# Kernel optimization log

Hardware: AMD Instinct MI355X
Metric: run time of the kernel (lower is better)

Reference implementation:

```python
import jax, jax.numpy as jnp
import numpy as np

B, N, H, F = 4, 512, 4096, 11008   # batch, seq, hidden, intermediate
L, R, RANK = 1, 16, 16             # layers stored, num adapters, lora rank
SCALE = 0.5                        # lora_scale


def setup_inputs() -> dict:
    key = jax.random.key(0)
    ks = jax.random.split(key, 12)
    nrm = lambda k, shape, fan: (jax.random.normal(k, shape, jnp.float32) * (fan ** -0.5))
    inp = {
        "x": jax.random.normal(ks[0], (B, N, H), jnp.float32),
        "W_gate": nrm(ks[1], (F, H), H),
        "W_up": nrm(ks[2], (F, H), H),
        "W_down": nrm(ks[3], (H, F), F),
        # LoRA tables: [num_layers, num_adapters, rank, in] and [num_layers, num_adapters, out, rank]
        "A_gate": nrm(ks[4], (L, R, RANK, H), H),
        "B_gate": nrm(ks[5], (L, R, F, RANK), RANK),
        "A_up": nrm(ks[6], (L, R, RANK, H), H),
        "B_up": nrm(ks[7], (L, R, F, RANK), RANK),
        "A_down": nrm(ks[8], (L, R, RANK, F), F),
        "B_down": nrm(ks[9], (L, R, H, RANK), RANK),
        "lora_indices": jax.random.randint(ks[10], (B,), 0, R),
        "layer_idx": 0,
    }
    return inp


def reference(x, W_gate, W_up, W_down, A_gate, B_gate, A_up, B_up,
              A_down, B_down, lora_indices, layer_idx):
    def lora_add(base, inp, A, B):
        # gather per-sequence adapter slices, then rank-r batched matmuls
        Ab = A[layer_idx][lora_indices]  # [B, r, in]
        Bb = B[layer_idx][lora_indices]  # [B, out, r]
        t = jnp.einsum('bri,bni->bnr', Ab, inp)        # down-project to rank
        return base + jnp.einsum('bor,bnr->bno', Bb, t) * SCALE

    gate = lora_add(jnp.einsum('bnh,fh->bnf', x, W_gate), x, A_gate, B_gate)
    up = lora_add(jnp.einsum('bnh,fh->bnf', x, W_up), x, A_up, B_up)
    act = jax.nn.silu(gate) * up                        # SwiGLU
    down = lora_add(jnp.einsum('bnf,hf->bnh', act, W_down), act, A_down, B_down)
    return down
```

## Files before the change

kernel.cpp:

```cpp
#include <hip/hip_runtime.h>
#include <hip/hip_bf16.h>

typedef __bf16 bf16x8 __attribute__((ext_vector_type(8)));
typedef float  f32x4  __attribute__((ext_vector_type(4)));
typedef unsigned short u16;

#define GLDS16(gsrc, ldst)                                                        \
  __builtin_amdgcn_global_load_lds(                                               \
      (const __attribute__((address_space(1))) unsigned int*)(gsrc),              \
      (__attribute__((address_space(3))) unsigned int*)(ldst), 16, 0, 0)

#define BAR() __builtin_amdgcn_s_barrier()
#define WAIT_LGKM0() asm volatile("s_waitcnt lgkmcnt(0)" ::: "memory")
#define WAIT_VM4() asm volatile("s_waitcnt vmcnt(4)" ::: "memory")

__device__ __forceinline__ u16 f2b(float f) {
  unsigned int u = __builtin_bit_cast(unsigned int, f);
  u = (u + 0x7fffu + ((u >> 16) & 1u)) >> 16;
  return (u16)u;
}
__device__ __forceinline__ float b2f(u16 b) {
  unsigned int u = ((unsigned int)b) << 16;
  return __builtin_bit_cast(float, u);
}

__global__ __launch_bounds__(256) void cvt_kernel(const float4* __restrict__ in,
                                                  ushort4* __restrict__ out, int n4) {
  int i = blockIdx.x * blockDim.x + threadIdx.x;
  int stride = gridDim.x * blockDim.x;
  for (; i < n4; i += stride) {
    float4 v = in[i];
    ushort4 o;
    o.x = f2b(v.x); o.y = f2b(v.y); o.z = f2b(v.z); o.w = f2b(v.w);
    out[i] = o;
  }
}

__global__ __launch_bounds__(256) void lora_t2(const u16* __restrict__ Xb, int K,
                                               const float* __restrict__ A1,
                                               const float* __restrict__ A2,
                                               const int* __restrict__ lidx,
                                               const int* __restrict__ layer,
                                               u16* __restrict__ t1,
                                               u16* __restrict__ t2) {
  __shared__ float red1[4][64][4];
  __shared__ float red2[4][64][4];
  const int lane = threadIdx.x & 63, wid = threadIdx.x >> 6;
  const int m0 = blockIdx.x * 16;
  const int li = lidx[m0 >> 9];
  const size_t abase = ((size_t)layer[0] * 16 + li) * 16 * (size_t)K;
  const int r = lane & 15, kg = lane >> 4;
  const int Kq = K >> 2, kb = wid * Kq;
  f32x4 acc1 = {0.f, 0.f, 0.f, 0.f}, acc2 = {0.f, 0.f, 0.f, 0.f};
  for (int k0 = kb; k0 < kb + Kq; k0 += 32) {
    bf16x8 a = *(const bf16x8*)&Xb[(size_t)(m0 + r) * K + k0 + kg * 8];
    const float* ap = A1 + abase + (size_t)r * K + k0 + kg * 8;
    float4 f0 = *(const float4*)ap;
    float4 f1 = *(const float4*)(ap + 4);
    bf16x8 b;
    b[0] = (__bf16)f0.x; b[1] = (__bf16)f0.y; b[2] = (__bf16)f0.z; b[3] = (__bf16)f0.w;
    b[4] = (__bf16)f1.x; b[5] = (__bf16)f1.y; b[6] = (__bf16)f1.z; b[7] = (__bf16)f1.w;
    acc1 = __builtin_amdgcn_mfma_f32_16x16x32_bf16(a, b, acc1, 0, 0, 0);
    if (A2) {
      const float* ap2 = A2 + abase + (size_t)r * K + k0 + kg * 8;
      float4 g0 = *(const float4*)ap2;
      float4 g1 = *(const float4*)(ap2 + 4);
      bf16x8 b2;
      b2[0] = (__bf16)g0.x; b2[1] = (__bf16)g0.y; b2[2] = (__bf16)g0.z; b2[3] = (__bf16)g0.w;
      b2[4] = (__bf16)g1.x; b2[5] = (__bf16)g1.y; b2[6] = (__bf16)g1.z; b2[7] = (__bf16)g1.w;
      acc2 = __builtin_amdgcn_mfma_f32_16x16x32_bf16(a, b2, acc2, 0, 0, 0);
    }
  }
#pragma unroll
  for (int j = 0; j < 4; ++j) {
    red1[wid][lane][j] = acc1[j];
    if (A2) red2[wid][lane][j] = acc2[j];
  }
  __syncthreads();
  if (wid == 0) {
#pragma unroll
    for (int j = 0; j < 4; ++j) {
      int m = m0 + kg * 4 + j;
      float v1 = red1[0][lane][j] + red1[1][lane][j] + red1[2][lane][j] + red1[3][lane][j];
      t1[(size_t)m * 16 + r] = f2b(0.5f * v1);
      if (A2) {
        float v2 = red2[0][lane][j] + red2[1][lane][j] + red2[2][lane][j] + red2[3][lane][j];
        t2[(size_t)m * 16 + r] = f2b(0.5f * v2);
      }
    }
  }
}

#define RD_A(dst, buf, mh) do {                                                \
    _Pragma("unroll")                                                          \
    for (int mf_ = 0; mf_ < 4; ++mf_)                                          \
      _Pragma("unroll")                                                        \
      for (int ks_ = 0; ks_ < 2; ++ks_) {                                      \
        int row_ = wm * 128 + (mh) * 64 + mf_ * 16 + lr;                       \
        int sl_ = (ks_ * 4 + kg) ^ rx;                                         \
        dst[mf_][ks_] = *(const bf16x8*)&sA[(buf) * 16384 + row_ * 64 + sl_ * 8]; \
      }                                                                        \
  } while (0)

#define RD_B(dst, buf, nh) do {                                                \
    _Pragma("unroll")                                                          \
    for (int nf_ = 0; nf_ < 2; ++nf_)                                          \
      _Pragma("unroll")                                                        \
      for (int ks_ = 0; ks_ < 2; ++ks_) {                                      \
        int row_ = wn * 64 + (nh) * 32 + nf_ * 16 + lr;                        \
        int sl_ = (ks_ * 4 + kg) ^ rx;                                         \
        dst[nf_][ks_] = *(const bf16x8*)&sB[(buf) * 16384 + row_ * 64 + sl_ * 8]; \
      }                                                                        \
  } while (0)

#define RD_BW(dst, SB, buf) do {                                               \
    _Pragma("unroll")                                                          \
    for (int nf_ = 0; nf_ < 2; ++nf_)                                          \
      _Pragma("unroll")                                                        \
      for (int ks_ = 0; ks_ < 2; ++ks_) {                                      \
        int row_ = wn * 32 + nf_ * 16 + lr;                                    \
        int sl_ = (ks_ * 4 + kg) ^ rx;                                         \
        dst[nf_][ks_] = *(const bf16x8*)&SB[(buf) * 8192 + row_ * 64 + sl_ * 8]; \
      }                                                                        \
  } while (0)

#define MMA_Q(AF, BF, mb, nb) do {                                             \
    __builtin_amdgcn_s_setprio(1);                                             \
    _Pragma("unroll")                                                          \
    for (int mf_ = 0; mf_ < 4; ++mf_)                                          \
      _Pragma("unroll")                                                        \
      for (int nf_ = 0; nf_ < 2; ++nf_)                                        \
        _Pragma("unroll")                                                      \
        for (int ks_ = 0; ks_ < 2; ++ks_)                                      \
          acc[(mb) + mf_][(nb) + nf_] = __builtin_amdgcn_mfma_f32_16x16x32_bf16( \
              AF[mf_][ks_], BF[nf_][ks_], acc[(mb) + mf_][(nb) + nf_], 0, 0, 0); \
    __builtin_amdgcn_s_setprio(0);                                             \
  } while (0)

#define MMA_F(AF, BF, ACC, mb) do {                                            \
    __builtin_amdgcn_s_setprio(1);                                             \
    _Pragma("unroll")                                                          \
    for (int mf_ = 0; mf_ < 4; ++mf_)                                          \
      _Pragma("unroll")                                                        \
      for (int nf_ = 0; nf_ < 2; ++nf_)                                        \
        _Pragma("unroll")                                                      \
        for (int ks_ = 0; ks_ < 2; ++ks_)                                      \
          ACC[(mb) + mf_][nf_] = __builtin_amdgcn_mfma_f32_16x16x32_bf16(      \
              AF[mf_][ks_], BF[nf_][ks_], ACC[(mb) + mf_][nf_], 0, 0, 0);      \
    __builtin_amdgcn_s_setprio(0);                                             \
  } while (0)

#define STAGE_F(buf, half, kt) do {                                            \
    const u16* gs_; u16* ld_;                                                  \
    if ((half) == 0)      { gs_ = Xb + (size_t)m0 * 4096 + (size_t)(kt) * 64;         ld_ = sA  + (buf) * 16384; }        \
    else if ((half) == 1) { gs_ = Xb + (size_t)(m0 + 128) * 4096 + (size_t)(kt) * 64; ld_ = sA  + (buf) * 16384 + 8192; } \
    else if ((half) == 2) { gs_ = Wg + (size_t)n0 * 4096 + (size_t)(kt) * 64;         ld_ = sBG + (buf) * 8192; }         \
    else                  { gs_ = Wu + (size_t)n0 * 4096 + (size_t)(kt) * 64;         ld_ = sBU + (buf) * 8192; }         \
    _Pragma("unroll")                                                          \
    for (int i_ = 0; i_ < 2; ++i_) {                                           \
      int ub_ = (wid << 6) + i_ * 512;                                         \
      int un_ = ub_ + lane;                                                    \
      int ur_ = un_ >> 3, us_ = (un_ & 7) ^ (ur_ & 7);                         \
      GLDS16(gs_ + (size_t)ur_ * 4096 + us_ * 8, ld_ + ub_ * 8);               \
    }                                                                          \
  } while (0)

__global__ __launch_bounds__(512, 2) void gemm_gup_fused(
    const u16* __restrict__ Xb, const u16* __restrict__ Wg, const u16* __restrict__ Wu,
    const u16* __restrict__ tg, const u16* __restrict__ tu,
    const float* __restrict__ Bg, const float* __restrict__ Bu,
    const int* __restrict__ lidx, const int* __restrict__ layer,
    u16* __restrict__ act,
    const float4* __restrict__ Wdf, ushort4* __restrict__ wdb3) {
  constexpr int F = 11008;
  const int b = blockIdx.x;
  if (b >= 704) {
    int i = (b - 704) * 512 + threadIdx.x;
    for (; i < 11272192; i += 256 * 512) {
      float4 v = Wdf[i];
      ushort4 o;
      o.x = f2b(v.x); o.y = f2b(v.y); o.z = f2b(v.z); o.w = f2b(v.w);
      wdb3[i] = o;
    }
    return;
  }
  const int xcd = b & 7, j = b >> 3;
  const int ny = xcd + 8 * (j >> 3);
  const int mx = j & 7;
  if (ny >= 86) return;
  extern __shared__ u16 smem[];
  u16* sA  = smem;
  u16* sBG = smem + 32768;
  u16* sBU = smem + 49152;
  const int tid = threadIdx.x, lane = tid & 63, wid = tid >> 6;
  const int lr = lane & 15, kg = lane >> 4, rx = lr & 7;
  const int wm = wid >> 2, wn = wid & 3;
  const int m0 = mx * 256;
  const int n0 = ny * 128;

  f32x4 accg[8][2] = {}, accu[8][2] = {};
  bf16x8 a0[4][2], a1[4][2], bg[2][2], bu[2][2];

  STAGE_F(0, 0, 0); STAGE_F(0, 1, 0); STAGE_F(0, 2, 0); STAGE_F(0, 3, 0);
  STAGE_F(1, 2, 1); STAGE_F(1, 3, 1);
  WAIT_VM4(); BAR();

#pragma unroll 1
  for (int u = 0; u < 32; ++u) {
    const int ktA = (2 * u + 1) & 63;
    const int kt0 = (2 * u + 2) & 63;
    const int kt1 = (2 * u + 3) & 63;
    RD_A(a0, 0, 0); RD_BW(bg, sBG, 0);
    STAGE_F(1, 0, ktA);
    BAR(); WAIT_LGKM0();
    MMA_F(a0, bg, accg, 0);
    BAR();
    RD_BW(bu, sBU, 0);
    STAGE_F(1, 1, ktA);
    BAR(); WAIT_LGKM0();
    MMA_F(a0, bu, accu, 0);
    BAR();
    RD_A(a1, 0, 1);
    STAGE_F(0, 2, kt0);
    BAR(); WAIT_LGKM0();
    MMA_F(a1, bu, accu, 4);
    BAR();
    STAGE_F(0, 3, kt0);
    BAR();
    MMA_F(a1, bg, accg, 4);
    WAIT_VM4();
    BAR();
    RD_A(a0, 1, 0); RD_BW(bg, sBG, 1);
    STAGE_F(0, 0, kt0);
    BAR(); WAIT_LGKM0();
    MMA_F(a0, bg, accg, 0);
    BAR();
    RD_BW(bu, sBU, 1);
    STAGE_F(0, 1, kt0);
    BAR(); WAIT_LGKM0();
    MMA_F(a0, bu, accu, 0);
    BAR();
    RD_A(a1, 1, 1);
    STAGE_F(1, 2, kt1);
    BAR(); WAIT_LGKM0();
    MMA_F(a1, bu, accu, 4);
    BAR();
    STAGE_F(1, 3, kt1);
    BAR();
    MMA_F(a1, bg, accg, 4);
    WAIT_VM4();
    BAR();
  }

  const int li = lidx[m0 >> 9];
  const size_t bbase = ((size_t)layer[0] * 16 + li) * (size_t)F * 16;
  bf16x8 la[8], lb[2];
  const bf16x8 zz = {};
#pragma unroll
  for (int mf = 0; mf < 8; ++mf) {
    int row = m0 + wm * 128 + mf * 16 + lr;
    la[mf] = (kg < 2) ? *(const bf16x8*)&tg[(size_t)row * 16 + kg * 8] : zz;
  }
#pragma unroll
  for (int nf = 0; nf < 2; ++nf) {
    int col = n0 + wn * 32 + nf * 16 + lr;
    if (kg < 2) {
      const float* bp = Bg + bbase + (size_t)col * 16 + kg * 8;
      float4 f0 = *(const float4*)bp;
      float4 f1 = *(const float4*)(bp + 4);
      bf16x8 v;
      v[0] = (__bf16)f0.x; v[1] = (__bf16)f0.y; v[2] = (__bf16)f0.z; v[3] = (__bf16)f0.w;
      v[4] = (__bf16)f1.x; v[5] = (__bf16)f1.y; v[6] = (__bf16)f1.z; v[7] = (__bf16)f1.w;
      lb[nf] = v;
    } else lb[nf] = zz;
  }
#pragma unroll
  for (int mf = 0; mf < 8; ++mf)
#pragma unroll
    for (int nf = 0; nf < 2; ++nf)
      accg[mf][nf] = __builtin_amdgcn_mfma_f32_16x16x32_bf16(la[mf], lb[nf], accg[mf][nf], 0, 0, 0);
#pragma unroll
  for (int mf = 0; mf < 8; ++mf) {
    int row = m0 + wm * 128 + mf * 16 + lr;
    la[mf] = (kg < 2) ? *(const bf16x8*)&tu[(size_t)row * 16 + kg * 8] : zz;
  }
#pragma unroll
  for (int nf = 0; nf < 2; ++nf) {
    int col = n0 + wn * 32 + nf * 16 + lr;
    if (kg < 2) {
      const float* bp = Bu + bbase + (size_t)col * 16 + kg * 8;
      float4 f0 = *(const float4*)bp;
      float4 f1 = *(const float4*)(bp + 4);
      bf16x8 v;
      v[0] = (__bf16)f0.x; v[1] = (__bf16)f0.y; v[2] = (__bf16)f0.z; v[3] = (__bf16)f0.w;
      v[4] = (__bf16)f1.x; v[5] = (__bf16)f1.y; v[6] = (__bf16)f1.z; v[7] = (__bf16)f1.w;
      lb[nf] = v;
    } else lb[nf] = zz;
  }
#pragma unroll
  for (int mf = 0; mf < 8; ++mf)
#pragma unroll
    for (int nf = 0; nf < 2; ++nf)
      accu[mf][nf] = __builtin_amdgcn_mfma_f32_16x16x32_bf16(la[mf], lb[nf], accu[mf][nf], 0, 0, 0);

#pragma unroll
  for (int mf = 0; mf < 8; ++mf)
#pragma unroll
    for (int nf = 0; nf < 2; ++nf)
#pragma unroll
      for (int j2 = 0; j2 < 4; ++j2) {
        int row = m0 + wm * 128 + mf * 16 + kg * 4 + j2;
        int col = n0 + wn * 32 + nf * 16 + lr;
        float g = accg[mf][nf][j2], uu = accu[mf][nf][j2];
        float s = g / (1.f + __expf(-g));
        act[(size_t)row * F + col] = f2b(s * uu);
      }
}

#define STAGE_D(buf, half, kt) do {                                           \
    int r0_ = ((half) & 1) * 128;                                             \
    const u16* gs_ = ((half) < 2)                                             \
        ? (Ab + (size_t)(m0 + r0_) * 11008 + (size_t)(kt) * 64)               \
        : (Wd + (size_t)(n0 + r0_) * 11008 + (size_t)(kt) * 64);              \
    u16* ld_ = (((half) < 2) ? sA : sB) + (buf) * 16384 + r0_ * 64;           \
    _Pragma("unroll")                                                         \
    for (int i_ = 0; i_ < 2; ++i_) {                                          \
      int ub_ = (wid << 6) + i_ * 512;                                        \
      int un_ = ub_ + lane;                                                   \
      int ur_ = un_ >> 3, us_ = (un_ & 7) ^ (ur_ & 7);                        \
      GLDS16(gs_ + (size_t)ur_ * 11008 + us_ * 8, ld_ + ub_ * 8);             \
    }                                                                         \
  } while (0)

#define KT(t) (kbase + ((t) >= 86 ? (t) - 86 : (t)))

__global__ __launch_bounds__(512, 2) void gemm_down8(
    const u16* __restrict__ Ab, const u16* __restrict__ Wd,
    const u16* __restrict__ td, const float* __restrict__ Bd,
    const int* __restrict__ lidx, const int* __restrict__ layer,
    float* __restrict__ P0, float* __restrict__ P1) {
  constexpr int H = 4096;
  extern __shared__ u16 smem[];
  u16* sA = smem;
  u16* sB = smem + 32768;
  const int tid = threadIdx.x, lane = tid & 63, wid = tid >> 6;
  const int lr = lane & 15, kg = lane >> 4, rx = lr & 7;
  const int wm = wid >> 2, wn = wid & 3;
  const int m0 = blockIdx.x * 256, n0 = blockIdx.y * 256;
  const int kbase = blockIdx.z * 86;
  float* P = blockIdx.z ? P1 : P0;

  f32x4 acc[8][4] = {};
  bf16x8 a0[4][2], a1[4][2], b0[2][2], b1[2][2];

  STAGE_D(0, 0, KT(0)); STAGE_D(0, 1, KT(0)); STAGE_D(0, 2, KT(0)); STAGE_D(0, 3, KT(0));
  STAGE_D(1, 2, KT(1)); STAGE_D(1, 3, KT(1));
  WAIT_VM4(); BAR();

#pragma unroll 1
  for (int u = 0; u < 43; ++u) {
    const int ktA = KT(2 * u + 1);
    const int kt0 = KT(2 * u + 2);
    const int kt1 = KT(2 * u + 3);
    RD_A(a0, 0, 0); RD_B(b0, 0, 0);
    STAGE_D(1, 0, ktA);
    BAR(); WAIT_LGKM0();
    MMA_Q(a0, b0, 0, 0);
    BAR();
    RD_B(b1, 0, 1);
    STAGE_D(1, 1, ktA);
    BAR(); WAIT_LGKM0();
    MMA_Q(a0, b1, 0, 2);
    BAR();
    RD_A(a1, 0, 1);
    STAGE_D(0, 2, kt0);
    BAR(); WAIT_LGKM0();
    MMA_Q(a1, b1, 4, 2);
    BAR();
    STAGE_D(0, 3, kt0);
    BAR();
    MMA_Q(a1, b0, 4, 0);
    WAIT_VM4();
    BAR();
    RD_A(a0, 1, 0); RD_B(b0, 1, 0);
    STAGE_D(0, 0, kt0);
    BAR(); WAIT_LGKM0();
    MMA_Q(a0, b0, 0, 0);
    BAR();
    RD_B(b1, 1, 1);
    STAGE_D(0, 1, kt0);
    BAR(); WAIT_LGKM0();
    MMA_Q(a0, b1, 0, 2);
    BAR();
    RD_A(a1, 1, 1);
    STAGE_D(1, 2, kt1);
    BAR(); WAIT_LGKM0();
    MMA_Q(a1, b1, 4, 2);
    BAR();
    STAGE_D(1, 3, kt1);
    BAR();
    MMA_Q(a1, b0, 4, 0);
    WAIT_VM4();
    BAR();
  }

  if (blockIdx.z == 0) {
    const int li = lidx[m0 >> 9];
    const size_t bbase = ((size_t)layer[0] * 16 + li) * (size_t)H * 16;
    bf16x8 la[8], lb[4];
    const bf16x8 zz = {};
#pragma unroll
    for (int mf = 0; mf < 8; ++mf) {
      int row = m0 + wm * 128 + mf * 16 + lr;
      la[mf] = (kg < 2) ? *(const bf16x8*)&td[(size_t)row * 16 + kg * 8] : zz;
    }
#pragma unroll
    for (int nf = 0; nf < 4; ++nf) {
      int col = n0 + wn * 64 + nf * 16 + lr;
      if (kg < 2) {
        const float* bp = Bd + bbase + (size_t)col * 16 + kg * 8;
        float4 f0 = *(const float4*)bp;
        float4 f1 = *(const float4*)(bp + 4);
        bf16x8 v;
        v[0] = (__bf16)f0.x; v[1] = (__bf16)f0.y; v[2] = (__bf16)f0.z; v[3] = (__bf16)f0.w;
        v[4] = (__bf16)f1.x; v[5] = (__bf16)f1.y; v[6] = (__bf16)f1.z; v[7] = (__bf16)f1.w;
        lb[nf] = v;
      } else lb[nf] = zz;
    }
#pragma unroll
    for (int mf = 0; mf < 8; ++mf)
#pragma unroll
      for (int nf = 0; nf < 4; ++nf)
        acc[mf][nf] = __builtin_amdgcn_mfma_f32_16x16x32_bf16(la[mf], lb[nf], acc[mf][nf], 0, 0, 0);
  }

#pragma unroll
  for (int mf = 0; mf < 8; ++mf)
#pragma unroll
    for (int nf = 0; nf < 4; ++nf)
#pragma unroll
      for (int j = 0; j < 4; ++j) {
        int row = m0 + wm * 128 + mf * 16 + kg * 4 + j;
        int col = n0 + wn * 64 + nf * 16 + lr;
        P[(size_t)row * H + col] = acc[mf][nf][j];
      }
}

__global__ __launch_bounds__(256) void combine_down(
    const float4* __restrict__ P0, const float4* __restrict__ P1,
    float4* __restrict__ out) {
  int gid = blockIdx.x * 256 + threadIdx.x;
  float4 p0 = P0[gid], p1 = P1[gid];
  out[gid] = make_float4(p0.x + p1.x, p0.y + p1.y, p0.z + p1.z, p0.w + p1.w);
}

extern "C" void kernel_launch(void* const* d_in, const int* in_sizes, int n_in,
                              void* d_out, int out_size, void* d_ws, size_t ws_size,
                              hipStream_t stream) {
  const float* x  = (const float*)d_in[0];
  const float* Wg = (const float*)d_in[1];
  const float* Wu = (const float*)d_in[2];
  const float* Wd = (const float*)d_in[3];
  const float* Ag = (const float*)d_in[4];
  const float* Bg = (const float*)d_in[5];
  const float* Au = (const float*)d_in[6];
  const float* Bu = (const float*)d_in[7];
  const float* Ad = (const float*)d_in[8];
  const float* Bd = (const float*)d_in[9];
  const int* lidx = (const int*)d_in[10];
  const int* lay  = (const int*)d_in[11];
  float* out = (float*)d_out;

  char* ws = (char*)d_ws;
  u16*  xb   = (u16*)(ws + 0);
  u16*  wgb  = (u16*)(ws + 16777216);
  u16*  wub  = (u16*)(ws + 106954752);
  u16*  gbuf = (u16*)(ws + 197132288);
  u16*  tg   = (u16*)(ws + 287309824);
  u16*  tu   = (u16*)(ws + 287375360);
  u16*  td   = (u16*)(ws + 287440896);
  u16*  wdb3 = (u16*)(ws + 287506432);
  float* P0  = (float*)(ws + 242221056);
  float* P1  = (float*)wub;

  hipFuncSetAttribute(reinterpret_cast<const void*>(gemm_gup_fused),
                      hipFuncAttributeMaxDynamicSharedMemorySize, 131072);
  hipFuncSetAttribute(reinterpret_cast<const void*>(gemm_down8),
                      hipFuncAttributeMaxDynamicSharedMemorySize, 131072);

  cvt_kernel<<<1024, 256, 0, stream>>>((const float4*)x,  (ushort4*)xb,  8388608 / 4);
  cvt_kernel<<<2048, 256, 0, stream>>>((const float4*)Wg, (ushort4*)wgb, 45088768 / 4);
  cvt_kernel<<<2048, 256, 0, stream>>>((const float4*)Wu, (ushort4*)wub, 45088768 / 4);

  lora_t2<<<128, 256, 0, stream>>>(xb, 4096, Ag, Au, lidx, lay, tg, tu);

  gemm_gup_fused<<<dim3(960), 512, 131072, stream>>>(
      xb, wgb, wub, tg, tu, Bg, Bu, lidx, lay, gbuf,
      (const float4*)Wd, (ushort4*)wdb3);

  lora_t2<<<128, 256, 0, stream>>>(gbuf, 11008, Ad, nullptr, lidx, lay, td, nullptr);

  gemm_down8<<<dim3(8, 16, 2), 512, 131072, stream>>>(gbuf, wdb3, td, Bd, lidx, lay,
                                                      P0, P1);

  combine_down<<<8192, 256, 0, stream>>>((const float4*)P0, (const float4*)P1,
                                         (float4*)out);
}
```

Measured before the change: 734.0 us.

## Fuse fp32-to-bf16 weight conversion into gate/up GEMM staging

Drops the two standalone conversion kernels for W_gate and W_up. The fused gate/up GEMM now loads fp32 weight tiles into registers, converts them to bf16 and writes them into LDS, while X still uses direct global-to-LDS loads. This removes a full read and write pass over both large weight matrices. In exchange, the GEMM reads fp32 weights, twice the bytes, once per M-block, and uses a register staging path with full vmcnt(0) waits, which may reduce overlap inside the main loop.

Result: slower. 980.3 us (+33.6%).

```diff
diff --git a/kernel.cpp b/kernel.cpp
--- a/kernel.cpp
+++ b/kernel.cpp
@@ -12,6 +12,7 @@
 
 #define BAR() __builtin_amdgcn_s_barrier()
 #define WAIT_LGKM0() asm volatile("s_waitcnt lgkmcnt(0)" ::: "memory")
+#define WAIT_VM0() asm volatile("s_waitcnt vmcnt(0)" ::: "memory")
 #define WAIT_VM4() asm volatile("s_waitcnt vmcnt(4)" ::: "memory")
 
 __device__ __forceinline__ u16 f2b(float f) {
@@ -150,12 +151,9 @@
     __builtin_amdgcn_s_setprio(0);                                             \
   } while (0)
 
-#define STAGE_F(buf, half, kt) do {                                            \
-    const u16* gs_; u16* ld_;                                                  \
-    if ((half) == 0)      { gs_ = Xb + (size_t)m0 * 4096 + (size_t)(kt) * 64;         ld_ = sA  + (buf) * 16384; }        \
-    else if ((half) == 1) { gs_ = Xb + (size_t)(m0 + 128) * 4096 + (size_t)(kt) * 64; ld_ = sA  + (buf) * 16384 + 8192; } \
-    else if ((half) == 2) { gs_ = Wg + (size_t)n0 * 4096 + (size_t)(kt) * 64;         ld_ = sBG + (buf) * 8192; }         \
-    else                  { gs_ = Wu + (size_t)n0 * 4096 + (size_t)(kt) * 64;         ld_ = sBU + (buf) * 8192; }         \
+#define STAGE_A(buf, half, kt) do {                                            \
+    const u16* gs_ = Xb + (size_t)(m0 + (half) * 128) * 4096 + (size_t)(kt) * 64; \
+    u16* ld_ = sA + (buf) * 16384 + (half) * 8192;                             \
     _Pragma("unroll")                                                          \
     for (int i_ = 0; i_ < 2; ++i_) {                                           \
       int ub_ = (wid << 6) + i_ * 512;                                         \
@@ -165,8 +163,33 @@
     }                                                                          \
   } while (0)
 
+#define WLOAD(dst, Wf, kt) do {                                                \
+    _Pragma("unroll")                                                          \
+    for (int i_ = 0; i_ < 2; ++i_) {                                           \
+      int ub_ = (wid << 6) + i_ * 512;                                         \
+      int un_ = ub_ + lane;                                                    \
+      int ur_ = un_ >> 3, us_ = (un_ & 7) ^ (ur_ & 7);                         \
+      const float* sp_ = Wf + (size_t)(n0 + ur_) * 4096 + (size_t)(kt) * 64 + us_ * 8; \
+      dst[2 * i_]     = *(const float4*)sp_;                                   \
+      dst[2 * i_ + 1] = *(const float4*)(sp_ + 4);                             \
+    }                                                                          \
+  } while (0)
+
+#define WWRITE(SB, buf, src) do {                                              \
+    _Pragma("unroll")                                                          \
+    for (int i_ = 0; i_ < 2; ++i_) {                                           \
+      int un_ = (wid << 6) + i_ * 512 + lane;                                  \
+      bf16x8 v_;                                                               \
+      v_[0] = (__bf16)src[2 * i_].x; v_[1] = (__bf16)src[2 * i_].y;            \
+      v_[2] = (__bf16)src[2 * i_].z; v_[3] = (__bf16)src[2 * i_].w;            \
+      v_[4] = (__bf16)src[2 * i_ + 1].x; v_[5] = (__bf16)src[2 * i_ + 1].y;    \
+      v_[6] = (__bf16)src[2 * i_ + 1].z; v_[7] = (__bf16)src[2 * i_ + 1].w;    \
+      *(bf16x8*)&SB[(buf) * 8192 + un_ * 8] = v_;                              \
+    }                                                                          \
+  } while (0)
+
 __global__ __launch_bounds__(512, 2) void gemm_gup_fused(
-    const u16* __restrict__ Xb, const u16* __restrict__ Wg, const u16* __restrict__ Wu,
+    const u16* __restrict__ Xb, const float* __restrict__ Wgf, const float* __restrict__ Wuf,
     const u16* __restrict__ tg, const u16* __restrict__ tu,
     const float* __restrict__ Bg, const float* __restrict__ Bu,
     const int* __restrict__ lidx, const int* __restrict__ layer,
@@ -200,10 +223,14 @@
 
   f32x4 accg[8][2] = {}, accu[8][2] = {};
   bf16x8 a0[4][2], a1[4][2], bg[2][2], bu[2][2];
-
-  STAGE_F(0, 0, 0); STAGE_F(0, 1, 0); STAGE_F(0, 2, 0); STAGE_F(0, 3, 0);
-  STAGE_F(1, 2, 1); STAGE_F(1, 3, 1);
-  WAIT_VM4(); BAR();
+  float4 wgv[4], wuv[4];
+
+  STAGE_A(0, 0, 0); STAGE_A(0, 1, 0);
+  WLOAD(wgv, Wgf, 0); WLOAD(wuv, Wuf, 0);
+  WWRITE(sBG, 0, wgv); WWRITE(sBU, 0, wuv);
+  WLOAD(wgv, Wgf, 1); WLOAD(wuv, Wuf, 1);
+  WWRITE(sBG, 1, wgv); WWRITE(sBU, 1, wuv);
+  WAIT_VM0(); WAIT_LGKM0(); BAR();
 
 #pragma unroll 1
   for (int u = 0; u < 32; ++u) {
@@ -211,44 +238,46 @@
     const int kt0 = (2 * u + 2) & 63;
     const int kt1 = (2 * u + 3) & 63;
     RD_A(a0, 0, 0); RD_BW(bg, sBG, 0);
-    STAGE_F(1, 0, ktA);
+    STAGE_A(1, 0, ktA); STAGE_A(1, 1, ktA);
+    WLOAD(wgv, Wgf, kt0);
     BAR(); WAIT_LGKM0();
     MMA_F(a0, bg, accg, 0);
     BAR();
     RD_BW(bu, sBU, 0);
-    STAGE_F(1, 1, ktA);
+    WLOAD(wuv, Wuf, kt0);
     BAR(); WAIT_LGKM0();
     MMA_F(a0, bu, accu, 0);
     BAR();
     RD_A(a1, 0, 1);
-    STAGE_F(0, 2, kt0);
+    WWRITE(sBG, 0, wgv);
     BAR(); WAIT_LGKM0();
     MMA_F(a1, bu, accu, 4);
     BAR();
-    STAGE_F(0, 3, kt0);
+    WWRITE(sBU, 0, wuv);
     BAR();
     MMA_F(a1, bg, accg, 4);
-    WAIT_VM4();
+    WAIT_VM0();
     BAR();
     RD_A(a0, 1, 0); RD_BW(bg, sBG, 1);
-    STAGE_F(0, 0, kt0);
+    STAGE_A(0, 0, kt0); STAGE_A(0, 1, kt0);
+    WLOAD(wgv, Wgf, kt1);
     BAR(); WAIT_LGKM0();
     MMA_F(a0, bg, accg, 0);
     BAR();
     RD_BW(bu, sBU, 1);
-    STAGE_F(0, 1, kt0);
+    WLOAD(wuv, Wuf, kt1);
     BAR(); WAIT_LGKM0();
     MMA_F(a0, bu, accu, 0);
     BAR();
     RD_A(a1, 1, 1);
-    STAGE_F(1, 2, kt1);
+    WWRITE(sBG, 1, wgv);
     BAR(); WAIT_LGKM0();
     MMA_F(a1, bu, accu, 4);
     BAR();
-    STAGE_F(1, 3, kt1);
+    WWRITE(sBU, 1, wuv);
     BAR();
     MMA_F(a1, bg, accg, 4);
-    WAIT_VM4();
+    WAIT_VM0();
     BAR();
   }
 
@@ -473,29 +502,25 @@
 
   char* ws = (char*)d_ws;
   u16*  xb   = (u16*)(ws + 0);
-  u16*  wgb  = (u16*)(ws + 16777216);
-  u16*  wub  = (u16*)(ws + 106954752);
+  float* P1  = (float*)(ws + 16777216);
   u16*  gbuf = (u16*)(ws + 197132288);
   u16*  tg   = (u16*)(ws + 287309824);
   u16*  tu   = (u16*)(ws + 287375360);
   u16*  td   = (u16*)(ws + 287440896);
   u16*  wdb3 = (u16*)(ws + 287506432);
   float* P0  = (float*)(ws + 242221056);
-  float* P1  = (float*)wub;
 
   hipFuncSetAttribute(reinterpret_cast<const void*>(gemm_gup_fused),
                       hipFuncAttributeMaxDynamicSharedMemorySize, 131072);
   hipFuncSetAttribute(reinterpret_cast<const void*>(gemm_down8),
                       hipFuncAttributeMaxDynamicSharedMemorySize, 131072);
 
-  cvt_kernel<<<1024, 256, 0, stream>>>((const float4*)x,  (ushort4*)xb,  8388608 / 4);
-  cvt_kernel<<<2048, 256, 0, stream>>>((const float4*)Wg, (ushort4*)wgb, 45088768 / 4);
-  cvt_kernel<<<2048, 256, 0, stream>>>((const float4*)Wu, (ushort4*)wub, 45088768 / 4);
+  cvt_kernel<<<1024, 256, 0, stream>>>((const float4*)x, (ushort4*)xb, 8388608 / 4);
 
   lora_t2<<<128, 256, 0, stream>>>(xb, 4096, Ag, Au, lidx, lay, tg, tu);
 
   gemm_gup_fused<<<dim3(960), 512, 131072, stream>>>(
-      xb, wgb, wub, tg, tu, Bg, Bu, lidx, lay, gbuf,
+      xb, Wg, Wu, tg, tu, Bg, Bu, lidx, lay, gbuf,
       (const float4*)Wd, (ushort4*)wdb3);
 
   lora_t2<<<128, 256, 0, stream>>>(gbuf, 11008, Ad, nullptr, lidx, lay, td, nullptr);
```
